# Kernel tuning notes

Hardware: AMD Instinct MI355X
Metric: run time of the kernel (lower is better)

Reference implementation:

```python
import jax, jax.numpy as jnp
import numpy as np
import math

B, N, D = 16, 1024, 1024

def setup_inputs() -> dict:
    key = jax.random.key(0)
    k1, k2, k3, k4 = jax.random.split(key, 4)
    x = jax.random.normal(k1, (B, N, D), dtype=jnp.float32)
    # Keras 'random_normal' initializer defaults to stddev=0.05
    w_keys = jax.random.normal(k2, (N, N), dtype=jnp.float32) * 0.05
    w_queries = jax.random.normal(k3, (N, N), dtype=jnp.float32) * 0.05
    w_values = jax.random.normal(k4, (N, N), dtype=jnp.float32) * 0.05
    return {"x": x, "w_keys": w_keys, "w_queries": w_queries, "w_values": w_values}

def reference(x, w_keys, w_queries, w_values):
    # x: (B, N, D); weights: (N, N); fact = sqrt(N) per build(input_shape[1])
    fact = math.sqrt(x.shape[1])
    ip = jnp.swapaxes(x, 1, 2)              # (B, D, N)
    vk = ip @ w_keys                         # (B, D, N)
    vq = ip @ w_queries                      # (B, D, N)
    vv = ip @ w_values                       # (B, D, N)
    kq = jnp.einsum('bdn,ben->bde', vk, vq) / fact   # (B, D, D)
    sm = jax.nn.softmax(kq, axis=-1)         # softmax over last axis
    # tf: sm @ transpose(pm(vv)) == sm @ vv  since pm then transpose_b cancel
    out = jnp.einsum('bde,ben->bdn', sm, vv) # (B, D, N)
    return jnp.swapaxes(out, 1, 2)           # (B, N, D)
```

## Files before the change

kernel.cpp:

```cpp
#include <hip/hip_runtime.h>
#include <stdint.h>


typedef __bf16 bf16x8_t __attribute__((ext_vector_type(8)));
typedef float  f32x4_t  __attribute__((ext_vector_type(4)));

typedef __attribute__((address_space(3))) uint32_t as3_u32;
typedef __attribute__((address_space(1))) uint32_t as1_u32;

__device__ __forceinline__ void async_copy16(const void* g, const void* l) {
  __builtin_amdgcn_global_load_lds((const as1_u32*)(uintptr_t)g,
                                   (as3_u32*)(uint32_t)(uintptr_t)l,
                                   16, 0, 0);
}

__device__ __forceinline__ uint16_t f2bf(float f) {
  uint32_t x = __float_as_uint(f);
  return (uint16_t)((x + 0x7fffu + ((x >> 16) & 1u)) >> 16);
}
__device__ __forceinline__ float bf2f(uint16_t b) {
  return __uint_as_float(((uint32_t)b) << 16);
}

template <bool OUT_F32>
__global__ __launch_bounds__(256, 4)
void gemm_bt(const uint16_t* __restrict__ A, const uint16_t* __restrict__ B,
             void* __restrict__ Cv, int K, int ldc,
             size_t sA, size_t sB, size_t sC, float alpha)
{
  __shared__ __align__(16) char smem[32768];
  char* As = smem;
  char* Bs = smem + 16384;

  const int lid  = blockIdx.x;
  const int xcd  = lid & 7;
  const int slot = lid >> 3;
  const int z    = (xcd << 1) | (slot >> 6);
  const int t64  = slot & 63;
  const int bm0  = (t64 >> 3) << 7;
  const int bn0  = (t64 & 7) << 7;

  A += (size_t)z * sA;
  B += (size_t)z * sB;

  const int t    = threadIdx.x;
  const int lane = t & 63;
  const int w    = t >> 6;
  const int q    = lane >> 4;
  const int r16  = lane & 15;
  const int wm   = (w >> 1) << 6;
  const int wn   = (w & 1) << 6;

  f32x4_t acc[4][4];
#pragma unroll
  for (int i = 0; i < 4; i++)
#pragma unroll
    for (int j = 0; j < 4; j++) acc[i][j] = (f32x4_t){0.f, 0.f, 0.f, 0.f};

  for (int k0 = 0; k0 < K; k0 += 64) {
#pragma unroll
    for (int i = 0; i < 4; i++) {
      const int o  = (i << 12) + (t << 4);
      const int m  = o >> 7;
      const int cp = (o >> 4) & 7;
      const int c  = cp ^ (m & 7);
      async_copy16(A + (size_t)(bm0 + m) * K + (size_t)(k0 + (c << 3)), As + o);
      async_copy16(B + (size_t)(bn0 + m) * K + (size_t)(k0 + (c << 3)), Bs + o);
    }
    __syncthreads();

#pragma unroll
    for (int kk = 0; kk < 2; kk++) {
      bf16x8_t af[4], bfr[4];
#pragma unroll
      for (int mi = 0; mi < 4; mi++) {
        const int m = wm + (mi << 4) + r16;
        const int c = (kk << 2) + q;
        af[mi] = *(const bf16x8_t*)(As + (m << 7) + ((c ^ (m & 7)) << 4));
      }
#pragma unroll
      for (int ni = 0; ni < 4; ni++) {
        const int n = wn + (ni << 4) + r16;
        const int c = (kk << 2) + q;
        bfr[ni] = *(const bf16x8_t*)(Bs + (n << 7) + ((c ^ (n & 7)) << 4));
      }
#pragma unroll
      for (int mi = 0; mi < 4; mi++)
#pragma unroll
        for (int ni = 0; ni < 4; ni++)
          acc[mi][ni] = __builtin_amdgcn_mfma_f32_16x16x32_bf16(
              af[mi], bfr[ni], acc[mi][ni], 0, 0, 0);
    }
    __syncthreads();
  }

  if (OUT_F32) {
    float* C = (float*)Cv + (size_t)z * sC;
#pragma unroll
    for (int mi = 0; mi < 4; mi++)
#pragma unroll
      for (int ni = 0; ni < 4; ni++)
#pragma unroll
        for (int r = 0; r < 4; r++) {
          const int row = bm0 + wm + (mi << 4) + (q << 2) + r;
          const int col = bn0 + wn + (ni << 4) + r16;
          C[(size_t)row * ldc + col] = acc[mi][ni][r] * alpha;
        }
  } else {
    float* reg = (float*)smem + (size_t)w * (16 * 66);
    uint16_t* C = (uint16_t*)Cv + (size_t)z * sC;
#pragma unroll
    for (int mi = 0; mi < 4; mi++) {
#pragma unroll
      for (int ni = 0; ni < 4; ni++)
#pragma unroll
        for (int r = 0; r < 4; r++)
          reg[((q << 2) + r) * 66 + (ni << 4) + r16] = acc[mi][ni][r] * alpha;
#pragma unroll
      for (int it = 0; it < 8; it++) {
        const int rr = (it << 1) + (lane >> 5);
        const int cc = (lane & 31) << 1;
        const float2 v = *(const float2*)(reg + rr * 66 + cc);
        const uint32_t p = (uint32_t)f2bf(v.x) | ((uint32_t)f2bf(v.y) << 16);
        const int row = bm0 + wm + (mi << 4) + rr;
        const int col = bn0 + wn + cc;
        *(uint32_t*)(C + (size_t)row * ldc + col) = p;
      }
    }
  }
}

__global__ __launch_bounds__(256)
void transpose_cast(const float* __restrict__ src, uint16_t* __restrict__ dst,
                    int R, int Ccols, size_t sStride, size_t dStride)
{
  __shared__ float tile[32][33];
  const int z = blockIdx.z;
  src += (size_t)z * sStride;
  dst += (size_t)z * dStride;
  const int c0 = blockIdx.x << 5;
  const int r0 = blockIdx.y << 5;
  const int tx = threadIdx.x;
  const int ty = threadIdx.y;
#pragma unroll
  for (int i = 0; i < 32; i += 8)
    tile[ty + i][tx] = src[(size_t)(r0 + ty + i) * Ccols + (c0 + tx)];
  __syncthreads();
#pragma unroll
  for (int i = 0; i < 32; i += 8)
    dst[(size_t)(c0 + ty + i) * R + (r0 + tx)] = f2bf(tile[tx][ty + i]);
}

__global__ __launch_bounds__(256)
void transpose_cast_w(const float* __restrict__ w0, const float* __restrict__ w1,
                      const float* __restrict__ w2, uint16_t* __restrict__ o0,
                      uint16_t* __restrict__ o1, uint16_t* __restrict__ o2)
{
  __shared__ float tile[32][33];
  const int z = blockIdx.z;
  const float* src = (z == 0) ? w0 : (z == 1) ? w1 : w2;
  uint16_t* dst = (z == 0) ? o0 : (z == 1) ? o1 : o2;
  const int c0 = blockIdx.x << 5;
  const int r0 = blockIdx.y << 5;
  const int tx = threadIdx.x;
  const int ty = threadIdx.y;
#pragma unroll
  for (int i = 0; i < 32; i += 8)
    tile[ty + i][tx] = src[(size_t)(r0 + ty + i) * 1024 + (c0 + tx)];
  __syncthreads();
#pragma unroll
  for (int i = 0; i < 32; i += 8)
    dst[(size_t)(c0 + ty + i) * 1024 + (r0 + tx)] = f2bf(tile[tx][ty + i]);
}

__global__ __launch_bounds__(256)
void softmax_rows(const uint16_t* __restrict__ in, uint16_t* __restrict__ out)
{
  const size_t row = blockIdx.x;
  const ushort4* p4 = (const ushort4*)(in + row * 1024);
  ushort4* o4 = (ushort4*)(out + row * 1024);
  const int t = threadIdx.x;
  const int lane = t & 63;
  const int wv = t >> 6;

  const ushort4 u = p4[t];
  float v0 = bf2f(u.x), v1 = bf2f(u.y), v2 = bf2f(u.z), v3 = bf2f(u.w);

  float m = fmaxf(fmaxf(v0, v1), fmaxf(v2, v3));
#pragma unroll
  for (int s = 32; s; s >>= 1) m = fmaxf(m, __shfl_xor(m, s, 64));
  __shared__ float red[8];
  if (lane == 0) red[wv] = m;
  __syncthreads();
  m = fmaxf(fmaxf(red[0], red[1]), fmaxf(red[2], red[3]));

  const float e0 = __expf(v0 - m), e1 = __expf(v1 - m);
  const float e2 = __expf(v2 - m), e3 = __expf(v3 - m);
  float s = e0 + e1 + e2 + e3;
#pragma unroll
  for (int sh = 32; sh; sh >>= 1) s += __shfl_xor(s, sh, 64);
  if (lane == 0) red[4 + wv] = s;
  __syncthreads();
  s = red[4] + red[5] + red[6] + red[7];

  const float inv = 1.0f / s;
  ushort4 r;
  r.x = f2bf(e0 * inv); r.y = f2bf(e1 * inv);
  r.z = f2bf(e2 * inv); r.w = f2bf(e3 * inv);
  o4[t] = r;
}

extern "C" void kernel_launch(void* const* d_in, const int* in_sizes, int n_in,
                              void* d_out, int out_size, void* d_ws, size_t ws_size,
                              hipStream_t stream)
{
  const float* x  = (const float*)d_in[0];
  const float* wk = (const float*)d_in[1];
  const float* wq = (const float*)d_in[2];
  const float* wv = (const float*)d_in[3];
  float* out = (float*)d_out;

  constexpr int BB = 16, N = 1024, D = 1024;
  constexpr size_t DN = (size_t)D * N;

  char* ws = (char*)d_ws;
  uint16_t* xT  = (uint16_t*)(ws);
  uint16_t* Wtk = (uint16_t*)(ws + (32ull << 20));
  uint16_t* Wtq = (uint16_t*)(ws + (34ull << 20));
  uint16_t* Wtv = (uint16_t*)(ws + (36ull << 20));
  uint16_t* vk  = (uint16_t*)(ws + (38ull << 20));
  uint16_t* vq  = (uint16_t*)(ws + (70ull << 20));
  uint16_t* vvT = (uint16_t*)(ws + (102ull << 20));
  uint16_t* kq  = xT;
  uint16_t* sm  = vk;

  const dim3 tb(32, 8);
  transpose_cast<<<dim3(D / 32, N / 32, BB), tb, 0, stream>>>(x, xT, N, D, DN, DN);
  transpose_cast_w<<<dim3(N / 32, N / 32, 3), tb, 0, stream>>>(wk, wq, wv,
                                                               Wtk, Wtq, Wtv);

  gemm_bt<false><<<1024, 256, 0, stream>>>(xT, Wtk, vk, 1024, 1024, DN, 0, DN, 1.0f);
  gemm_bt<false><<<1024, 256, 0, stream>>>(xT, Wtq, vq, 1024, 1024, DN, 0, DN, 1.0f);
  gemm_bt<false><<<1024, 256, 0, stream>>>(Wtv, xT, vvT, 1024, 1024, 0, DN, DN, 1.0f);
  gemm_bt<false><<<1024, 256, 0, stream>>>(vk, vq, kq, 1024, 1024, DN, DN, DN, 0.03125f);
  softmax_rows<<<BB * D, 256, 0, stream>>>(kq, sm);
  gemm_bt<true><<<1024, 256, 0, stream>>>(vvT, sm, out, 1024, 1024, DN, DN, DN, 1.0f);
}
```

Before: 335.9 us.

## Use 32x32x16 MFMA, batch projection GEMMs into one launch, merge transposes

Switches the GEMM inner loop from 16x16x32 to 32x32x16 bf16 MFMA tiles, with a 2x2 fragment grid per wave and a matching epilogue remap. The three projection GEMMs are folded into one grouped launch of 3072 blocks, and the x and weight transpose-cast kernels are merged into a single launch. The aim is fewer LDS fragment reads per MFMA and less launch and tail overhead. Shared memory grows slightly because the 32-row per-wave epilogue staging needs more space.

```diff
diff --git a/kernel.cpp b/kernel.cpp
--- a/kernel.cpp
+++ b/kernel.cpp
@@ -2,8 +2,8 @@
 #include <stdint.h>
 
 
-typedef __bf16 bf16x8_t __attribute__((ext_vector_type(8)));
-typedef float  f32x4_t  __attribute__((ext_vector_type(4)));
+typedef __bf16 bf16x8_t  __attribute__((ext_vector_type(8)));
+typedef float  f32x16_t  __attribute__((ext_vector_type(16)));
 
 typedef __attribute__((address_space(3))) uint32_t as3_u32;
 typedef __attribute__((address_space(1))) uint32_t as1_u32;
@@ -22,40 +22,48 @@
   return __uint_as_float(((uint32_t)b) << 16);
 }
 
-template <bool OUT_F32>
+struct G3 {
+  const uint16_t* A[3]; const uint16_t* B[3]; void* C[3];
+  size_t sA[3], sB[3], sC[3]; float alpha[3];
+};
+
+template <bool OUT_F32, int NG>
 __global__ __launch_bounds__(256, 4)
-void gemm_bt(const uint16_t* __restrict__ A, const uint16_t* __restrict__ B,
-             void* __restrict__ Cv, int K, int ldc,
-             size_t sA, size_t sB, size_t sC, float alpha)
-{
-  __shared__ __align__(16) char smem[32768];
+void gemm_bt(G3 ga, int K, int ldc)
+{
+  __shared__ __align__(16) char smem[33792];
   char* As = smem;
   char* Bs = smem + 16384;
 
-  const int lid  = blockIdx.x;
-  const int xcd  = lid & 7;
-  const int slot = lid >> 3;
+  const int lid = blockIdx.x;
+  const int g   = (NG == 1) ? 0 : (lid >> 10);
+  const int l   = lid & 1023;
+  const int xcd  = l & 7;
+  const int slot = l >> 3;
   const int z    = (xcd << 1) | (slot >> 6);
   const int t64  = slot & 63;
   const int bm0  = (t64 >> 3) << 7;
   const int bn0  = (t64 & 7) << 7;
 
-  A += (size_t)z * sA;
-  B += (size_t)z * sB;
+  const uint16_t* A = ga.A[g] + (size_t)z * ga.sA[g];
+  const uint16_t* B = ga.B[g] + (size_t)z * ga.sB[g];
+  const float alpha = ga.alpha[g];
 
   const int t    = threadIdx.x;
   const int lane = t & 63;
   const int w    = t >> 6;
-  const int q    = lane >> 4;
-  const int r16  = lane & 15;
+  const int l32  = lane & 31;
+  const int kh   = lane >> 5;
   const int wm   = (w >> 1) << 6;
   const int wn   = (w & 1) << 6;
 
-  f32x4_t acc[4][4];
-#pragma unroll
-  for (int i = 0; i < 4; i++)
-#pragma unroll
-    for (int j = 0; j < 4; j++) acc[i][j] = (f32x4_t){0.f, 0.f, 0.f, 0.f};
+  f32x16_t acc[2][2];
+#pragma unroll
+  for (int i = 0; i < 2; i++)
+#pragma unroll
+    for (int j = 0; j < 2; j++)
+#pragma unroll
+      for (int r = 0; r < 16; r++) acc[i][j][r] = 0.f;
 
   for (int k0 = 0; k0 < K; k0 += 64) {
 #pragma unroll
@@ -70,59 +78,60 @@
     __syncthreads();
 
 #pragma unroll
-    for (int kk = 0; kk < 2; kk++) {
-      bf16x8_t af[4], bfr[4];
-#pragma unroll
-      for (int mi = 0; mi < 4; mi++) {
-        const int m = wm + (mi << 4) + r16;
-        const int c = (kk << 2) + q;
-        af[mi] = *(const bf16x8_t*)(As + (m << 7) + ((c ^ (m & 7)) << 4));
+    for (int s = 0; s < 4; s++) {
+      const int cidx = (s << 1) | kh;
+      bf16x8_t af[2], bfr[2];
+#pragma unroll
+      for (int mi = 0; mi < 2; mi++) {
+        const int m = wm + (mi << 5) + l32;
+        af[mi] = *(const bf16x8_t*)(As + (m << 7) + ((cidx ^ (m & 7)) << 4));
       }
 #pragma unroll
-      for (int ni = 0; ni < 4; ni++) {
-        const int n = wn + (ni << 4) + r16;
-        const int c = (kk << 2) + q;
-        bfr[ni] = *(const bf16x8_t*)(Bs + (n << 7) + ((c ^ (n & 7)) << 4));
+      for (int ni = 0; ni < 2; ni++) {
+        const int n = wn + (ni << 5) + l32;
+        bfr[ni] = *(const bf16x8_t*)(Bs + (n << 7) + ((cidx ^ (n & 7)) << 4));
       }
 #pragma unroll
-      for (int mi = 0; mi < 4; mi++)
-#pragma unroll
-        for (int ni = 0; ni < 4; ni++)
-          acc[mi][ni] = __builtin_amdgcn_mfma_f32_16x16x32_bf16(
+      for (int mi = 0; mi < 2; mi++)
+#pragma unroll
+        for (int ni = 0; ni < 2; ni++)
+          acc[mi][ni] = __builtin_amdgcn_mfma_f32_32x32x16_bf16(
               af[mi], bfr[ni], acc[mi][ni], 0, 0, 0);
     }
     __syncthreads();
   }
 
   if (OUT_F32) {
-    float* C = (float*)Cv + (size_t)z * sC;
-#pragma unroll
-    for (int mi = 0; mi < 4; mi++)
-#pragma unroll
-      for (int ni = 0; ni < 4; ni++)
-#pragma unroll
-        for (int r = 0; r < 4; r++) {
-          const int row = bm0 + wm + (mi << 4) + (q << 2) + r;
-          const int col = bn0 + wn + (ni << 4) + r16;
+    float* C = (float*)ga.C[g] + (size_t)z * ga.sC[g];
+#pragma unroll
+    for (int mi = 0; mi < 2; mi++)
+#pragma unroll
+      for (int ni = 0; ni < 2; ni++)
+#pragma unroll
+        for (int r = 0; r < 16; r++) {
+          const int row = bm0 + wm + (mi << 5) + (r & 3) + ((r >> 2) << 3) + (kh << 2);
+          const int col = bn0 + wn + (ni << 5) + l32;
           C[(size_t)row * ldc + col] = acc[mi][ni][r] * alpha;
         }
   } else {
-    float* reg = (float*)smem + (size_t)w * (16 * 66);
-    uint16_t* C = (uint16_t*)Cv + (size_t)z * sC;
-#pragma unroll
-    for (int mi = 0; mi < 4; mi++) {
-#pragma unroll
-      for (int ni = 0; ni < 4; ni++)
-#pragma unroll
-        for (int r = 0; r < 4; r++)
-          reg[((q << 2) + r) * 66 + (ni << 4) + r16] = acc[mi][ni][r] * alpha;
-#pragma unroll
-      for (int it = 0; it < 8; it++) {
-        const int rr = (it << 1) + (lane >> 5);
-        const int cc = (lane & 31) << 1;
+    float* reg = (float*)smem + (size_t)w * (32 * 66);
+    uint16_t* C = (uint16_t*)ga.C[g] + (size_t)z * ga.sC[g];
+#pragma unroll
+    for (int mi = 0; mi < 2; mi++) {
+#pragma unroll
+      for (int ni = 0; ni < 2; ni++)
+#pragma unroll
+        for (int r = 0; r < 16; r++) {
+          const int row32 = (r & 3) + ((r >> 2) << 3) + (kh << 2);
+          reg[row32 * 66 + (ni << 5) + l32] = acc[mi][ni][r] * alpha;
+        }
+#pragma unroll
+      for (int it = 0; it < 16; it++) {
+        const int rr = (it << 1) | kh;
+        const int cc = l32 << 1;
         const float2 v = *(const float2*)(reg + rr * 66 + cc);
         const uint32_t p = (uint32_t)f2bf(v.x) | ((uint32_t)f2bf(v.y) << 16);
-        const int row = bm0 + wm + (mi << 4) + rr;
+        const int row = bm0 + wm + (mi << 5) + rr;
         const int col = bn0 + wn + cc;
         *(uint32_t*)(C + (size_t)row * ldc + col) = p;
       }
@@ -131,35 +140,21 @@
 }
 
 __global__ __launch_bounds__(256)
-void transpose_cast(const float* __restrict__ src, uint16_t* __restrict__ dst,
-                    int R, int Ccols, size_t sStride, size_t dStride)
+void transpose_cast_all(const float* __restrict__ x,
+                        const float* __restrict__ wk,
+                        const float* __restrict__ wq,
+                        const float* __restrict__ wv,
+                        uint16_t* __restrict__ xT, uint16_t* __restrict__ Wtk,
+                        uint16_t* __restrict__ Wtq, uint16_t* __restrict__ Wtv)
 {
   __shared__ float tile[32][33];
   const int z = blockIdx.z;
-  src += (size_t)z * sStride;
-  dst += (size_t)z * dStride;
-  const int c0 = blockIdx.x << 5;
-  const int r0 = blockIdx.y << 5;
-  const int tx = threadIdx.x;
-  const int ty = threadIdx.y;
-#pragma unroll
-  for (int i = 0; i < 32; i += 8)
-    tile[ty + i][tx] = src[(size_t)(r0 + ty + i) * Ccols + (c0 + tx)];
-  __syncthreads();
-#pragma unroll
-  for (int i = 0; i < 32; i += 8)
-    dst[(size_t)(c0 + ty + i) * R + (r0 + tx)] = f2bf(tile[tx][ty + i]);
-}
-
-__global__ __launch_bounds__(256)
-void transpose_cast_w(const float* __restrict__ w0, const float* __restrict__ w1,
-                      const float* __restrict__ w2, uint16_t* __restrict__ o0,
-                      uint16_t* __restrict__ o1, uint16_t* __restrict__ o2)
-{
-  __shared__ float tile[32][33];
-  const int z = blockIdx.z;
-  const float* src = (z == 0) ? w0 : (z == 1) ? w1 : w2;
-  uint16_t* dst = (z == 0) ? o0 : (z == 1) ? o1 : o2;
+  const float* src;
+  uint16_t* dst;
+  if (z < 16)      { src = x + (size_t)z * 1048576; dst = xT + (size_t)z * 1048576; }
+  else if (z == 16){ src = wk; dst = Wtk; }
+  else if (z == 17){ src = wq; dst = Wtq; }
+  else             { src = wv; dst = Wtv; }
   const int c0 = blockIdx.x << 5;
   const int r0 = blockIdx.y << 5;
   const int tx = threadIdx.x;
@@ -220,8 +215,8 @@
   const float* wv = (const float*)d_in[3];
   float* out = (float*)d_out;
 
-  constexpr int BB = 16, N = 1024, D = 1024;
-  constexpr size_t DN = (size_t)D * N;
+  constexpr int BB = 16;
+  constexpr size_t DN = 1048576;
 
   char* ws = (char*)d_ws;
   uint16_t* xT  = (uint16_t*)(ws);
@@ -234,15 +229,27 @@
   uint16_t* kq  = xT;
   uint16_t* sm  = vk;
 
-  const dim3 tb(32, 8);
-  transpose_cast<<<dim3(D / 32, N / 32, BB), tb, 0, stream>>>(x, xT, N, D, DN, DN);
-  transpose_cast_w<<<dim3(N / 32, N / 32, 3), tb, 0, stream>>>(wk, wq, wv,
-                                                               Wtk, Wtq, Wtv);
-
-  gemm_bt<false><<<1024, 256, 0, stream>>>(xT, Wtk, vk, 1024, 1024, DN, 0, DN, 1.0f);
-  gemm_bt<false><<<1024, 256, 0, stream>>>(xT, Wtq, vq, 1024, 1024, DN, 0, DN, 1.0f);
-  gemm_bt<false><<<1024, 256, 0, stream>>>(Wtv, xT, vvT, 1024, 1024, 0, DN, DN, 1.0f);
-  gemm_bt<false><<<1024, 256, 0, stream>>>(vk, vq, kq, 1024, 1024, DN, DN, DN, 0.03125f);
-  softmax_rows<<<BB * D, 256, 0, stream>>>(kq, sm);
-  gemm_bt<true><<<1024, 256, 0, stream>>>(vvT, sm, out, 1024, 1024, DN, DN, DN, 1.0f);
-}
+  transpose_cast_all<<<dim3(32, 32, 19), dim3(32, 8), 0, stream>>>(
+      x, wk, wq, wv, xT, Wtk, Wtq, Wtv);
+
+  G3 proj;
+  proj.A[0] = xT;  proj.B[0] = Wtk; proj.C[0] = vk;
+  proj.sA[0] = DN; proj.sB[0] = 0;  proj.sC[0] = DN; proj.alpha[0] = 1.0f;
+  proj.A[1] = xT;  proj.B[1] = Wtq; proj.C[1] = vq;
+  proj.sA[1] = DN; proj.sB[1] = 0;  proj.sC[1] = DN; proj.alpha[1] = 1.0f;
+  proj.A[2] = Wtv; proj.B[2] = xT;  proj.C[2] = vvT;
+  proj.sA[2] = 0;  proj.sB[2] = DN; proj.sC[2] = DN; proj.alpha[2] = 1.0f;
+  gemm_bt<false, 3><<<3072, 256, 0, stream>>>(proj, 1024, 1024);
+
+  G3 gkq = {};
+  gkq.A[0] = vk;  gkq.B[0] = vq; gkq.C[0] = kq;
+  gkq.sA[0] = DN; gkq.sB[0] = DN; gkq.sC[0] = DN; gkq.alpha[0] = 0.03125f;
+  gemm_bt<false, 1><<<1024, 256, 0, stream>>>(gkq, 1024, 1024);
+
+  softmax_rows<<<BB * 1024, 256, 0, stream>>>(kq, sm);
+
+  G3 gout = {};
+  gout.A[0] = vvT; gout.B[0] = sm; gout.C[0] = out;
+  gout.sA[0] = DN; gout.sB[0] = DN; gout.sC[0] = DN; gout.alpha[0] = 1.0f;
+  gemm_bt<true, 1><<<1024, 256, 0, stream>>>(gout, 1024, 1024);
+}
```

Result: no change. 336.1 us (+0.1%).
